# Kernel optimization log

Hardware: AMD Instinct MI355X
Metric: run time of the kernel (lower is better)

Reference implementation:

```python
import jax, jax.numpy as jnp
import numpy as np

B, N, D, H, DD = 4, 256, 768, 12, 64
HD = D // H  # head_dim = 64
SCALE = float(np.sqrt(HD))


def _layernorm(x, g, b, eps=1e-5):
    mu = jnp.mean(x, axis=-1, keepdims=True)
    var = jnp.var(x, axis=-1, keepdims=True)
    return (x - mu) / jnp.sqrt(var + eps) * g + b


def setup_inputs() -> dict:
    key = jax.random.key(0)
    ks = jax.random.split(key, 20)
    def w(k, shape, fan_in):
        return (jax.random.normal(k, shape, jnp.float32) / np.sqrt(fan_in)).astype(jnp.float32)
    x = jax.random.normal(ks[0], (B, N, D), jnp.float32)
    dist = jax.random.normal(ks[1], (B, N, N, DD), jnp.float32)
    mask = jax.random.randint(ks[2], (B, N, N), 0, 2) > 0
    eye = jnp.eye(N, dtype=bool)[None]
    edge_mask = jnp.logical_or(mask, eye)  # guarantee no fully-masked row
    return {
        'x': x, 'distance_features': dist, 'edge_mask': edge_mask,
        'qkv_w': w(ks[3], (D, 3 * D), D), 'qkv_b': jnp.zeros((3 * D,), jnp.float32),
        'out_w': w(ks[4], (D, D), D), 'out_b': jnp.zeros((D,), jnp.float32),
        'rb_w1': w(ks[5], (DD, D), DD), 'rb_b1': jnp.zeros((D,), jnp.float32),
        'rb_w2': w(ks[6], (D, H), D), 'rb_b2': jnp.zeros((H,), jnp.float32),
        'gate_w1': w(ks[7], (D, D), D), 'gate_b1': jnp.zeros((D,), jnp.float32),
        'gate_w2': w(ks[8], (D, D), D), 'gate_b2': jnp.zeros((D,), jnp.float32),
        'ff_w1': w(ks[9], (D, 2 * D), D), 'ff_b1': jnp.zeros((2 * D,), jnp.float32),
        'ff_w2': w(ks[10], (2 * D, D), 2 * D), 'ff_b2': jnp.zeros((D,), jnp.float32),
        'ln1_g': jnp.ones((D,), jnp.float32), 'ln1_b': jnp.zeros((D,), jnp.float32),
        'ln2_g': jnp.ones((D,), jnp.float32), 'ln2_b': jnp.zeros((D,), jnp.float32),
    }


def reference(x, distance_features, edge_mask, qkv_w, qkv_b, out_w, out_b,
              rb_w1, rb_b1, rb_w2, rb_b2, gate_w1, gate_b1, gate_w2, gate_b2,
              ff_w1, ff_b1, ff_w2, ff_b2, ln1_g, ln1_b, ln2_g, ln2_b):
    residual = x
    xn = _layernorm(x, ln1_g, ln1_b)
    qkv = xn @ qkv_w + qkv_b
    q, k, v = jnp.split(qkv, 3, axis=-1)
    q = q.reshape(B, N, H, HD)
    k = k.reshape(B, N, H, HD)
    v = v.reshape(B, N, H, HD)
    logits = jnp.einsum('bihd,bjhd->bhij', q, k) / SCALE
    bias = jax.nn.silu(distance_features @ rb_w1 + rb_b1) @ rb_w2 + rb_b2  # [B,N,N,H]
    logits = logits + jnp.transpose(bias, (0, 3, 1, 2))
    neg = jnp.finfo(logits.dtype).min
    logits = jnp.where(edge_mask[:, None, :, :], logits, neg)
    attn = jax.nn.softmax(logits, axis=-1)
    context = jnp.einsum('bhij,bjhd->bihd', attn, v).reshape(B, N, D)
    gated = jax.nn.silu(xn @ gate_w1 + gate_b1) @ gate_w2 + gate_b2
    x2 = residual + (context * jax.nn.sigmoid(gated)) @ out_w + out_b
    y = _layernorm(x2, ln2_g, ln2_b)
    ff = jax.nn.gelu(y @ ff_w1 + ff_b1, approximate=False) @ ff_w2 + ff_b2
    return x2 + ff
```

## Files before the change

### kernel.cpp

```cpp
#include <hip/hip_runtime.h>
#include <hip/hip_bf16.h>
#include <cmath>

#define U16 unsigned short

typedef __bf16 bf16x8_t __attribute__((ext_vector_type(8)));
typedef float f32x4_t __attribute__((ext_vector_type(4)));

union Frag { uint4 u4; unsigned u[4]; bf16x8_t b8; U16 s[8]; };

__device__ __forceinline__ float b2f(U16 u) {
  union { unsigned int i; float f; } x; x.i = ((unsigned int)u) << 16; return x.f;
}
__device__ __forceinline__ U16 f2b(float f) {
  union { float f; unsigned int i; } x; x.f = f;
  unsigned int r = x.i + 0x7FFFu + ((x.i >> 16) & 1u);
  return (U16)(r >> 16);
}
__device__ __forceinline__ unsigned cvt_pk_bf16(float a, float b) {
  union { __hip_bfloat162 h2; unsigned u; } x;
  x.h2 = __float22bfloat162_rn(make_float2(a, b));
  return x.u;
}
__device__ __forceinline__ float fast_silu(float z) {
  return z * __builtin_amdgcn_rcpf(1.f + __expf(-z));
}
__device__ __forceinline__ void load_lds16(const U16* g, U16* l) {
  __builtin_amdgcn_global_load_lds((const __attribute__((address_space(1))) void*)g,
                                   (__attribute__((address_space(3))) void*)l, 16, 0, 0);
}

__device__ __forceinline__ void ln_row(int row, const float* __restrict__ X,
                                       const float* __restrict__ gam,
                                       const float* __restrict__ bet,
                                       U16* __restrict__ Y) {
  int tid = threadIdx.x, lane = tid & 63, wave = tid >> 6;
  __shared__ float p1[4], p2[4];
  float v[3];
#pragma unroll
  for (int j = 0; j < 3; ++j) v[j] = X[(size_t)row * 768 + tid + j * 256];
  float s1 = v[0] + v[1] + v[2];
  float s2 = v[0] * v[0] + v[1] * v[1] + v[2] * v[2];
#pragma unroll
  for (int m = 32; m > 0; m >>= 1) {
    s1 += __shfl_xor(s1, m);
    s2 += __shfl_xor(s2, m);
  }
  if (lane == 0) { p1[wave] = s1; p2[wave] = s2; }
  __syncthreads();
  float t1 = p1[0] + p1[1] + p1[2] + p1[3];
  float t2 = p2[0] + p2[1] + p2[2] + p2[3];
  float mean = t1 * (1.f / 768.f);
  float var = t2 * (1.f / 768.f) - mean * mean;
  float rstd = rsqrtf(var + 1e-5f);
#pragma unroll
  for (int j = 0; j < 3; ++j) {
    int c = tid + j * 256;
    Y[(size_t)row * 768 + c] = f2b((v[j] - mean) * rstd * gam[c] + bet[c]);
  }
}

__global__ __launch_bounds__(256) void prep_kernel(
    const float* __restrict__ qkv_w, const float* __restrict__ out_w,
    const float* __restrict__ g1w, const float* __restrict__ g2w,
    const float* __restrict__ ff1w, const float* __restrict__ ff2w,
    const float* __restrict__ rb1w, const float* __restrict__ rb2w,
    const float* __restrict__ qkv_b, const float* __restrict__ gate_b1,
    U16* __restrict__ qkv_wT, U16* __restrict__ out_wT, U16* __restrict__ g1wT,
    U16* __restrict__ g2wT, U16* __restrict__ ff1wT, U16* __restrict__ ff2wT,
    U16* __restrict__ rb1wT, U16* __restrict__ rb2wL, float* __restrict__ qg_bias,
    const float* __restrict__ x, const float* __restrict__ ln1_g,
    const float* __restrict__ ln1_b, U16* __restrict__ xn) {
  int bid = blockIdx.x;
  if (bid >= 5868) {
    ln_row(bid - 5868, x, ln1_g, ln1_b, xn);
    return;
  }
  if (bid >= 5856) {
    int idx = (bid - 5856) * 256 + threadIdx.x;
    qg_bias[idx] = (idx < 2304) ? qkv_b[idx] : gate_b1[idx - 2304];
    return;
  }
  if (bid >= 5808) {
    int idx = (bid - 5808) * 256 + threadIdx.x;
    int j = idx & 7, lane = (idx >> 3) & 63, pp = idx >> 9;
    int row = lane & 15, col = pp * 32 + ((lane >> 4) << 3) + j;
    rb2wL[idx] = (row < 12) ? f2b(rb2w[col * 12 + row]) : (U16)0;
    return;
  }
  const float* in; U16* out; int R, C, base;
  if (bid < 1728)      { in = qkv_w; out = qkv_wT; R = 768;  C = 2304; base = 0; }
  else if (bid < 2304) { in = out_w; out = out_wT; R = 768;  C = 768;  base = 1728; }
  else if (bid < 2880) { in = g1w;   out = g1wT;   R = 768;  C = 768;  base = 2304; }
  else if (bid < 3456) { in = g2w;   out = g2wT;   R = 768;  C = 768;  base = 2880; }
  else if (bid < 4608) { in = ff1w;  out = ff1wT;  R = 768;  C = 1536; base = 3456; }
  else if (bid < 5760) { in = ff2w;  out = ff2wT;  R = 1536; C = 768;  base = 4608; }
  else                 { in = rb1w;  out = rb1wT;  R = 64;   C = 768;  base = 5760; }
  int bx = bid - base, tilesx = C / 32;
  int c0 = (bx % tilesx) * 32, r0 = (bx / tilesx) * 32;
  __shared__ float tile[32][33];
  int tx = threadIdx.x & 31, ty = threadIdx.x >> 5;
#pragma unroll
  for (int yy = 0; yy < 4; ++yy)
    tile[ty + yy * 8][tx] = in[(size_t)(r0 + ty + yy * 8) * C + c0 + tx];
  __syncthreads();
#pragma unroll
  for (int yy = 0; yy < 4; ++yy)
    out[(size_t)(c0 + ty + yy * 8) * R + r0 + tx] = f2b(tile[tx][ty + yy * 8]);
}

template <int EPI, bool OUTF32>
__device__ __forceinline__ void gemm_core(U16* sA, U16* sB,
                                          const U16* __restrict__ A,
                                          const U16* __restrict__ BT,
                                          const float* __restrict__ bias,
                                          const float* __restrict__ other,
                                          void* __restrict__ Cout,
                                          float* __restrict__ Cout2,
                                          int N, int K, int bx, int by) {
  int tid = threadIdx.x;
  int lane = tid & 63, wave = tid >> 6;
  int m0 = by * 64, n0 = bx * 64;
  int wm = (wave >> 1) * 32, wn = (wave & 1) * 32;
  int lm = lane & 15, lq = lane >> 4;
  int srow = tid >> 2, scol = (tid & 3) * 8;
  const U16* ag = A + (size_t)(m0 + srow) * K + scol;
  const U16* bg = BT + (size_t)(n0 + srow) * K + scol;
  int nit = K >> 5;
  load_lds16(ag, sA + tid * 8);
  load_lds16(bg, sB + tid * 8);
  f32x4_t acc[2][2] = {};
  for (int i = 0; i < nit; ++i) {
    __syncthreads();
    int cb = (i & 1) * 2048, nb = ((i + 1) & 1) * 2048;
    if (i + 1 < nit) {
      load_lds16(ag + (i + 1) * 32, sA + nb + tid * 8);
      load_lds16(bg + (i + 1) * 32, sB + nb + tid * 8);
    }
    Frag af[2], bf[2];
#pragma unroll
    for (int mt = 0; mt < 2; ++mt)
      af[mt].u4 = *(const uint4*)&sA[cb + (wm + mt * 16 + lm) * 32 + lq * 8];
#pragma unroll
    for (int nt = 0; nt < 2; ++nt)
      bf[nt].u4 = *(const uint4*)&sB[cb + (wn + nt * 16 + lm) * 32 + lq * 8];
#pragma unroll
    for (int mt = 0; mt < 2; ++mt)
#pragma unroll
      for (int nt = 0; nt < 2; ++nt)
        acc[mt][nt] = __builtin_amdgcn_mfma_f32_16x16x32_bf16(af[mt].b8, bf[nt].b8,
                                                              acc[mt][nt], 0, 0, 0);
  }
#pragma unroll
  for (int nt = 0; nt < 2; ++nt) {
    int gc = n0 + wn + nt * 16 + lm;
    float bz = bias[gc];
#pragma unroll
    for (int mt = 0; mt < 2; ++mt) {
#pragma unroll
      for (int r = 0; r < 4; ++r) {
        int gr = m0 + wm + mt * 16 + lq * 4 + r;
        float z = acc[mt][nt][r] + bz;
        if (EPI == 5) {
          if (gc < 2304) Cout2[(size_t)gr * 2304 + gc] = z;
          else ((U16*)Cout)[(size_t)gr * 768 + gc - 2304] = f2b(fast_silu(z));
          continue;
        }
        size_t idx = (size_t)gr * N + gc;
        float o;
        if (EPI == 0) o = z;
        else if (EPI == 2) o = 0.5f * z * (1.f + erff(z * 0.70710678118f));
        else if (EPI == 6) o = __builtin_amdgcn_rcpf(1.f + __expf(-z));
        else o = z + other[idx];
        if (OUTF32) ((float*)Cout)[idx] = o;
        else ((U16*)Cout)[idx] = f2b(o);
      }
    }
  }
}

template <int EPI, bool OUTF32>
__global__ __launch_bounds__(256) void gemm_bt(const U16* __restrict__ A,
                                               const U16* __restrict__ BT,
                                               const float* __restrict__ bias,
                                               const float* __restrict__ other,
                                               void* __restrict__ Cout,
                                               int N, int K) {
  __shared__ __align__(16) U16 sA[2 * 2048];
  __shared__ __align__(16) U16 sB[2 * 2048];
  gemm_core<EPI, OUTF32>(sA, sB, A, BT, bias, other, Cout, nullptr, N, K,
                         blockIdx.x, blockIdx.y);
}

__device__ void rb_body(int bid, const float* __restrict__ dist,
                        const U16* __restrict__ w1T, const float* __restrict__ b1,
                        const U16* __restrict__ w2L, const float* __restrict__ b2,
                        float* __restrict__ biasOut) {
  int tid = threadIdx.x;
  int lane = tid & 63, wave = tid >> 6;
  int lm = lane & 15, lq = lane >> 4;
  int r0 = bid * 512;
  float hb = (lm < 12) ? b2[lm] : 0.f;
  Frag bd[8][2];
#pragma unroll
  for (int g = 0; g < 8; ++g) {
    const float* ap = dist + (size_t)(r0 + (wave * 8 + g) * 16 + lm) * 64 + lq * 8;
    float4 v0 = ((const float4*)ap)[0];
    float4 v1 = ((const float4*)ap)[1];
    float4 v2 = ((const float4*)(ap + 32))[0];
    float4 v3 = ((const float4*)(ap + 32))[1];
    bd[g][0].u[0] = cvt_pk_bf16(v0.x, v0.y); bd[g][0].u[1] = cvt_pk_bf16(v0.z, v0.w);
    bd[g][0].u[2] = cvt_pk_bf16(v1.x, v1.y); bd[g][0].u[3] = cvt_pk_bf16(v1.z, v1.w);
    bd[g][1].u[0] = cvt_pk_bf16(v2.x, v2.y); bd[g][1].u[1] = cvt_pk_bf16(v2.z, v2.w);
    bd[g][1].u[2] = cvt_pk_bf16(v3.x, v3.y); bd[g][1].u[3] = cvt_pk_bf16(v3.z, v3.w);
  }
  const U16* w1p0 = w1T + (size_t)(((lm >> 2) << 3) + (lm & 3)) * 64 + lq * 8;
  const U16* w1p1 = w1p0 + 256;
  const U16* w2p = w2L + lane * 8;
  const float* b1p = b1 + lq * 8;
  f32x4_t bacc[8];
#pragma unroll
  for (int g = 0; g < 8; ++g) bacc[g] = {hb, hb, hb, hb};

  auto loadw = [&](int j, Frag& f00, Frag& f01, Frag& f10, Frag& f11, Frag& fwb,
                   float4& fb0, float4& fb1) {
    const U16* p0 = w1p0 + (size_t)j * 2048;
    const U16* p1 = w1p1 + (size_t)j * 2048;
    f00.u4 = *(const uint4*)p0;
    f01.u4 = *(const uint4*)(p0 + 32);
    f10.u4 = *(const uint4*)p1;
    f11.u4 = *(const uint4*)(p1 + 32);
    fwb.u4 = *(const uint4*)(w2p + (size_t)j * 512);
    fb0 = *(const float4*)(b1p + j * 32);
    fb1 = *(const float4*)(b1p + j * 32 + 4);
  };
  auto comp = [&](Frag& f00, Frag& f01, Frag& f10, Frag& f11, Frag& fwb,
                  float4 fb0, float4 fb1) {
    f32x4_t cz0 = {fb0.x, fb0.y, fb0.z, fb0.w};
    f32x4_t cz1 = {fb1.x, fb1.y, fb1.z, fb1.w};
#pragma unroll
    for (int g = 0; g < 8; ++g) {
      f32x4_t z0 = cz0, z1 = cz1;
      z0 = __builtin_amdgcn_mfma_f32_16x16x32_bf16(f00.b8, bd[g][0].b8, z0, 0, 0, 0);
      z0 = __builtin_amdgcn_mfma_f32_16x16x32_bf16(f01.b8, bd[g][1].b8, z0, 0, 0, 0);
      z1 = __builtin_amdgcn_mfma_f32_16x16x32_bf16(f10.b8, bd[g][0].b8, z1, 0, 0, 0);
      z1 = __builtin_amdgcn_mfma_f32_16x16x32_bf16(f11.b8, bd[g][1].b8, z1, 0, 0, 0);
      float s0 = fast_silu(z0[0]), s1 = fast_silu(z0[1]);
      float s2 = fast_silu(z0[2]), s3 = fast_silu(z0[3]);
      float t0 = fast_silu(z1[0]), t1 = fast_silu(z1[1]);
      float t2 = fast_silu(z1[2]), t3 = fast_silu(z1[3]);
      Frag af2;
      af2.u[0] = cvt_pk_bf16(s0, s1); af2.u[1] = cvt_pk_bf16(s2, s3);
      af2.u[2] = cvt_pk_bf16(t0, t1); af2.u[3] = cvt_pk_bf16(t2, t3);
      bacc[g] = __builtin_amdgcn_mfma_f32_16x16x32_bf16(af2.b8, fwb.b8, bacc[g], 0, 0, 0);
    }
  };

  Frag e00, e01, e10, e11, ewb, o00, o01, o10, o11, owb;
  float4 eb0, eb1, ob0, ob1;
  loadw(0, e00, e01, e10, e11, ewb, eb0, eb1);
  for (int pp = 0; pp < 24; pp += 2) {
    loadw(pp + 1, o00, o01, o10, o11, owb, ob0, ob1);
    comp(e00, e01, e10, e11, ewb, eb0, eb1);
    if (pp + 2 < 24) loadw(pp + 2, e00, e01, e10, e11, ewb, eb0, eb1);
    comp(o00, o01, o10, o11, owb, ob0, ob1);
  }
  if (lm < 12) {
#pragma unroll
    for (int g = 0; g < 8; ++g) {
#pragma unroll
      for (int r = 0; r < 4; ++r) {
        int gr = r0 + (wave * 8 + g) * 16 + lq * 4 + r;
        int b = gr >> 16, rem = gr & 65535, i = rem >> 8, j = rem & 255;
        biasOut[(((size_t)b * 12 + lm) * 256 + i) * 256 + j] = bacc[g][r];
      }
    }
  }
}

__global__ __launch_bounds__(256) void qkvrb_kernel(
    const U16* __restrict__ xn, const U16* __restrict__ qg_wT,
    const float* __restrict__ qg_b, float* __restrict__ qkvb, U16* __restrict__ g1,
    const float* __restrict__ dist, const U16* __restrict__ rb1wT,
    const float* __restrict__ rb_b1, const U16* __restrict__ rb2wL,
    const float* __restrict__ rb_b2, float* __restrict__ biasB) {
  __shared__ __align__(16) U16 sA[2 * 2048];
  __shared__ __align__(16) U16 sB[2 * 2048];
  int bid = blockIdx.x;
  if (bid < 512) {
    rb_body(bid, dist, rb1wT, rb_b1, rb2wL, rb_b2, biasB);
  } else {
    int g = bid - 512;
    gemm_core<5, false>(sA, sB, xn, qg_wT, qg_b, nullptr, g1, qkvb, 3072, 768,
                        g % 48, g / 48);
  }
}

__device__ void attn_body(unsigned char* smem, int bid,
                          const float* __restrict__ qkv,
                          const float* __restrict__ biasB,
                          const int* __restrict__ mask,
                          float* __restrict__ ctx) {
  U16* sK = (U16*)smem;
  float(*sQ)[66] = (float(*)[66])(smem + 33024);
  float* sP = (float*)(smem + 33024 + 4224);
  int tid = threadIdx.x, lane = tid & 63, w = tid >> 6;
  int bh = bid >> 4, b = bh / 12, h = bh % 12;
  int i0 = (bid & 15) * 16;
  {
    int r = tid >> 4, c = (tid & 15) * 4;
    *(float4*)&sQ[r][c] =
        *(const float4*)&qkv[((size_t)(b * 256 + i0 + r)) * 2304 + h * 64 + c];
  }
  {
    const float* kr = qkv + ((size_t)(b * 256 + w * 64)) * 2304 + 768 + h * 64 + lane;
#pragma unroll 8
    for (int rr = 0; rr < 64; ++rr) {
      float kv = kr[(size_t)rr * 2304];
      sK[lane * 258 + w * 64 + rr] = (U16)cvt_pk_bf16(kv, kv);
    }
  }
  __syncthreads();
  int iw = i0 + w * 4;
  float lacc[4][4] = {};
#pragma unroll 4
  for (int d = 0; d < 64; ++d) {
    float k0 = b2f(sK[d * 258 + lane]);
    float k1 = b2f(sK[d * 258 + 64 + lane]);
    float k2 = b2f(sK[d * 258 + 128 + lane]);
    float k3 = b2f(sK[d * 258 + 192 + lane]);
#pragma unroll
    for (int qi = 0; qi < 4; ++qi) {
      float qv = sQ[w * 4 + qi][d];
      lacc[qi][0] += qv * k0;
      lacc[qi][1] += qv * k1;
      lacc[qi][2] += qv * k2;
      lacc[qi][3] += qv * k3;
    }
  }
#pragma unroll
  for (int qi = 0; qi < 4; ++qi) {
    int gi = iw + qi;
    const float* brow = biasB + (((size_t)b * 12 + h) * 256 + gi) * 256;
    const int* mrow = mask + ((size_t)b * 256 + gi) * 256;
    float lg[4];
#pragma unroll
    for (int jc = 0; jc < 4; ++jc) {
      float lv = lacc[qi][jc] * 0.125f + brow[jc * 64 + lane];
      lg[jc] = mrow[jc * 64 + lane] ? lv : -1e30f;
    }
    float mx = fmaxf(fmaxf(lg[0], lg[1]), fmaxf(lg[2], lg[3]));
#pragma unroll
    for (int m = 32; m > 0; m >>= 1) mx = fmaxf(mx, __shfl_xor(mx, m));
    float e[4], sum = 0.f;
#pragma unroll
    for (int jc = 0; jc < 4; ++jc) { e[jc] = __expf(lg[jc] - mx); sum += e[jc]; }
#pragma unroll
    for (int m = 32; m > 0; m >>= 1) sum += __shfl_xor(sum, m);
    float inv = __builtin_amdgcn_rcpf(sum);
#pragma unroll
    for (int jc = 0; jc < 4; ++jc) sP[(w * 4 + qi) * 256 + jc * 64 + lane] = e[jc] * inv;
  }
  float ca[4] = {0.f, 0.f, 0.f, 0.f};
  const float* vcol = qkv + (size_t)b * 256 * 2304 + 1536 + h * 64 + lane;
#pragma unroll 2
  for (int j4 = 0; j4 < 256; j4 += 4) {
    float4 p0 = *(const float4*)&sP[(w * 4 + 0) * 256 + j4];
    float4 p1 = *(const float4*)&sP[(w * 4 + 1) * 256 + j4];
    float4 p2 = *(const float4*)&sP[(w * 4 + 2) * 256 + j4];
    float4 p3 = *(const float4*)&sP[(w * 4 + 3) * 256 + j4];
    const float* pp0 = (const float*)&p0;
    const float* pp1 = (const float*)&p1;
    const float* pp2 = (const float*)&p2;
    const float* pp3 = (const float*)&p3;
#pragma unroll
    for (int jj = 0; jj < 4; ++jj) {
      float v = vcol[(size_t)(j4 + jj) * 2304];
      ca[0] += pp0[jj] * v;
      ca[1] += pp1[jj] * v;
      ca[2] += pp2[jj] * v;
      ca[3] += pp3[jj] * v;
    }
  }
#pragma unroll
  for (int qi = 0; qi < 4; ++qi)
    ctx[((size_t)(b * 256 + iw + qi)) * 768 + h * 64 + lane] = ca[qi];
}

__global__ __launch_bounds__(256) void attn_gate_kernel(
    const float* __restrict__ qkv, const float* __restrict__ biasB,
    const int* __restrict__ mask, float* __restrict__ ctx,
    const U16* __restrict__ g1, const U16* __restrict__ g2wT,
    const float* __restrict__ gate_b2, U16* __restrict__ sg) {
  __shared__ __align__(16) unsigned char smem[53632];
  int bid = blockIdx.x;
  if (bid < 768) {
    attn_body(smem, bid, qkv, biasB, mask, ctx);
  } else {
    int g = bid - 768;
    gemm_core<6, false>((U16*)smem, (U16*)(smem + 8192), g1, g2wT, gate_b2, nullptr,
                        sg, nullptr, 768, 768, g % 12, g / 12);
  }
}

__global__ __launch_bounds__(256) void outp_kernel(const float* __restrict__ ctx,
                                                   const U16* __restrict__ sg,
                                                   const U16* __restrict__ out_wT,
                                                   const float* __restrict__ out_b,
                                                   const float* __restrict__ x,
                                                   float* __restrict__ x2) {
  __shared__ __align__(16) U16 sA[64 * 32];
  __shared__ __align__(16) U16 sB[2 * 2048];
  int tid = threadIdx.x;
  int lane = tid & 63, wave = tid >> 6;
  int m0 = blockIdx.y * 64, n0 = blockIdx.x * 64;
  int wm = (wave >> 1) * 32, wn = (wave & 1) * 32;
  int lm = lane & 15, lq = lane >> 4;
  int srow = tid >> 2, scol = (tid & 3) * 8;
  const float* cg0 = ctx + (size_t)(m0 + srow) * 768 + scol;
  const U16* sg0 = sg + (size_t)(m0 + srow) * 768 + scol;
  const U16* bg = out_wT + (size_t)(n0 + srow) * 768 + scol;
  load_lds16(bg, sB + tid * 8);
  float4 ca0 = *(const float4*)cg0;
  float4 ca1 = *(const float4*)(cg0 + 4);
  Frag sa; sa.u4 = *(const uint4*)sg0;
  f32x4_t acc[2][2] = {};
  for (int i = 0; i < 24; ++i) {
    __syncthreads();
    int cb = (i & 1) * 2048, nb = ((i + 1) & 1) * 2048;
    if (i + 1 < 24) load_lds16(bg + (i + 1) * 32, sB + nb + tid * 8);
    Frag av;
    av.u[0] = cvt_pk_bf16(ca0.x * b2f(sa.s[0]), ca0.y * b2f(sa.s[1]));
    av.u[1] = cvt_pk_bf16(ca0.z * b2f(sa.s[2]), ca0.w * b2f(sa.s[3]));
    av.u[2] = cvt_pk_bf16(ca1.x * b2f(sa.s[4]), ca1.y * b2f(sa.s[5]));
    av.u[3] = cvt_pk_bf16(ca1.z * b2f(sa.s[6]), ca1.w * b2f(sa.s[7]));
    *(uint4*)&sA[tid * 8] = av.u4;
    if (i + 1 < 24) {
      ca0 = *(const float4*)(cg0 + (i + 1) * 32);
      ca1 = *(const float4*)(cg0 + (i + 1) * 32 + 4);
      sa.u4 = *(const uint4*)(sg0 + (i + 1) * 32);
    }
    __syncthreads();
    Frag af[2], bf[2];
#pragma unroll
    for (int mt = 0; mt < 2; ++mt)
      af[mt].u4 = *(const uint4*)&sA[(wm + mt * 16 + lm) * 32 + lq * 8];
#pragma unroll
    for (int nt = 0; nt < 2; ++nt)
      bf[nt].u4 = *(const uint4*)&sB[cb + (wn + nt * 16 + lm) * 32 + lq * 8];
#pragma unroll
    for (int mt = 0; mt < 2; ++mt)
#pragma unroll
      for (int nt = 0; nt < 2; ++nt)
        acc[mt][nt] = __builtin_amdgcn_mfma_f32_16x16x32_bf16(af[mt].b8, bf[nt].b8,
                                                              acc[mt][nt], 0, 0, 0);
  }
#pragma unroll
  for (int nt = 0; nt < 2; ++nt) {
    int gc = n0 + wn + nt * 16 + lm;
    float bz = out_b[gc];
#pragma unroll
    for (int mt = 0; mt < 2; ++mt) {
#pragma unroll
      for (int r = 0; r < 4; ++r) {
        int gr = m0 + wm + mt * 16 + lq * 4 + r;
        size_t idx = (size_t)gr * 768 + gc;
        x2[idx] = acc[mt][nt][r] + bz + x[idx];
      }
    }
  }
}

__global__ __launch_bounds__(256) void ln_kernel(const float* __restrict__ X,
                                                 const float* __restrict__ gam,
                                                 const float* __restrict__ bet,
                                                 U16* __restrict__ Y) {
  ln_row(blockIdx.x, X, gam, bet, Y);
}

extern "C" void kernel_launch(void* const* d_in, const int* in_sizes, int n_in,
                              void* d_out, int out_size, void* d_ws, size_t ws_size,
                              hipStream_t stream) {
  const float* x       = (const float*)d_in[0];
  const float* dist    = (const float*)d_in[1];
  const int* mask      = (const int*)d_in[2];
  const float* qkv_w   = (const float*)d_in[3];
  const float* qkv_b   = (const float*)d_in[4];
  const float* out_w   = (const float*)d_in[5];
  const float* out_b   = (const float*)d_in[6];
  const float* rb_w1   = (const float*)d_in[7];
  const float* rb_b1   = (const float*)d_in[8];
  const float* rb_w2   = (const float*)d_in[9];
  const float* rb_b2   = (const float*)d_in[10];
  const float* gate_w1 = (const float*)d_in[11];
  const float* gate_b1 = (const float*)d_in[12];
  const float* gate_w2 = (const float*)d_in[13];
  const float* gate_b2 = (const float*)d_in[14];
  const float* ff_w1   = (const float*)d_in[15];
  const float* ff_b1   = (const float*)d_in[16];
  const float* ff_w2   = (const float*)d_in[17];
  const float* ff_b2   = (const float*)d_in[18];
  const float* ln1_g   = (const float*)d_in[19];
  const float* ln1_b   = (const float*)d_in[20];
  const float* ln2_g   = (const float*)d_in[21];
  const float* ln2_b   = (const float*)d_in[22];

  char* w = (char*)d_ws;
  auto alloc = [&](size_t bytes) {
    char* p = w;
    w += (bytes + 255) & ~(size_t)255;
    return p;
  };
  U16* xn      = (U16*)alloc(1024 * 768 * 2);
  float* qkvb  = (float*)alloc((size_t)1024 * 2304 * 4);
  U16* qg_wT   = (U16*)alloc((size_t)3072 * 768 * 2);
  U16* qkv_wT  = qg_wT;
  U16* g1wT    = qg_wT + (size_t)2304 * 768;
  float* qg_b  = (float*)alloc(3072 * 4);
  U16* out_wT  = (U16*)alloc(768 * 768 * 2);
  U16* g2wT    = (U16*)alloc(768 * 768 * 2);
  U16* ff1wT   = (U16*)alloc(1536 * 768 * 2);
  U16* ff2wT   = (U16*)alloc(768 * 1536 * 2);
  U16* rb1wT   = (U16*)alloc(768 * 64 * 2);
  U16* rb2wL   = (U16*)alloc(24 * 64 * 8 * 2);
  float* biasB = (float*)alloc((size_t)4 * 12 * 256 * 256 * 4);
  float* ctx   = (float*)alloc(1024 * 768 * 4);
  U16* g1      = (U16*)alloc(1024 * 768 * 2);
  U16* sg      = (U16*)alloc(1024 * 768 * 2);
  float* x2    = (float*)alloc(1024 * 768 * 4);
  U16* y       = (U16*)alloc(1024 * 768 * 2);
  U16* f1      = (U16*)alloc(1024 * 1536 * 2);
  (void)ws_size; (void)in_sizes; (void)n_in; (void)out_size;

  prep_kernel<<<6892, 256, 0, stream>>>(qkv_w, out_w, gate_w1, gate_w2, ff_w1, ff_w2,
                                        rb_w1, rb_w2, qkv_b, gate_b1,
                                        qkv_wT, out_wT, g1wT, g2wT, ff1wT, ff2wT,
                                        rb1wT, rb2wL, qg_b, x, ln1_g, ln1_b, xn);
  qkvrb_kernel<<<1280, 256, 0, stream>>>(xn, qg_wT, qg_b, qkvb, g1,
                                         dist, rb1wT, rb_b1, rb2wL, rb_b2, biasB);
  attn_gate_kernel<<<960, 256, 0, stream>>>(qkvb, biasB, mask, ctx,
                                            g1, g2wT, gate_b2, sg);
  outp_kernel<<<dim3(12, 16), 256, 0, stream>>>(ctx, sg, out_wT, out_b, x, x2);
  ln_kernel<<<1024, 256, 0, stream>>>(x2, ln2_g, ln2_b, y);
  gemm_bt<2, false><<<dim3(24, 16), 256, 0, stream>>>(y, ff1wT, ff_b1, nullptr, f1,
                                                      1536, 768);
  gemm_bt<4, true><<<dim3(12, 16), 256, 0, stream>>>(f1, ff2wT, ff_b2, x2, (float*)d_out,
                                                     768, 1536);
}
```

Measured before the change: 318.2 us.

## Fuse all stages into a persistent megakernel with global atomic barriers

Replaces the seven separate kernel launches with one persistent kernel of 512 blocks. The blocks loop over each stage's work items and meet at software grid barriers built from atomic counters that are zeroed by a memset before the launch. This removes per-launch overhead and the idle gaps between kernels. In exchange it adds spin-wait barriers, and it depends on all 512 blocks being resident at once (two blocks per CU at 53 KB of LDS), otherwise it deadlocks. Later stages with few work items leave many blocks idle, and the restrict qualifiers are dropped.

```diff
diff --git a/kernel.cpp b/kernel.cpp
--- a/kernel.cpp
+++ b/kernel.cpp
@@ -30,12 +30,24 @@
                                    (__attribute__((address_space(3))) void*)l, 16, 0, 0);
 }
 
-__device__ __forceinline__ void ln_row(int row, const float* __restrict__ X,
-                                       const float* __restrict__ gam,
-                                       const float* __restrict__ bet,
-                                       U16* __restrict__ Y) {
+__device__ __forceinline__ void gbar(unsigned* cnt, int idx, unsigned nb) {
+  __syncthreads();
+  if (threadIdx.x == 0) {
+    __threadfence();
+    atomicAdd(&cnt[idx * 16], 1u);
+    while (__hip_atomic_load(&cnt[idx * 16], __ATOMIC_RELAXED,
+                             __HIP_MEMORY_SCOPE_AGENT) < nb)
+      __builtin_amdgcn_s_sleep(2);
+    __threadfence();
+  }
+  __syncthreads();
+}
+
+__device__ __forceinline__ void ln_row(int row, const float* X, const float* gam,
+                                       const float* bet, U16* Y) {
   int tid = threadIdx.x, lane = tid & 63, wave = tid >> 6;
   __shared__ float p1[4], p2[4];
+  __syncthreads();
   float v[3];
 #pragma unroll
   for (int j = 0; j < 3; ++j) v[j] = X[(size_t)row * 768 + tid + j * 256];
@@ -60,22 +72,15 @@
   }
 }
 
-__global__ __launch_bounds__(256) void prep_kernel(
-    const float* __restrict__ qkv_w, const float* __restrict__ out_w,
-    const float* __restrict__ g1w, const float* __restrict__ g2w,
-    const float* __restrict__ ff1w, const float* __restrict__ ff2w,
-    const float* __restrict__ rb1w, const float* __restrict__ rb2w,
-    const float* __restrict__ qkv_b, const float* __restrict__ gate_b1,
-    U16* __restrict__ qkv_wT, U16* __restrict__ out_wT, U16* __restrict__ g1wT,
-    U16* __restrict__ g2wT, U16* __restrict__ ff1wT, U16* __restrict__ ff2wT,
-    U16* __restrict__ rb1wT, U16* __restrict__ rb2wL, float* __restrict__ qg_bias,
-    const float* __restrict__ x, const float* __restrict__ ln1_g,
-    const float* __restrict__ ln1_b, U16* __restrict__ xn) {
-  int bid = blockIdx.x;
-  if (bid >= 5868) {
-    ln_row(bid - 5868, x, ln1_g, ln1_b, xn);
-    return;
-  }
+__device__ void prep_item(int bid, float* tile,
+                          const float* qkv_w, const float* out_w, const float* g1w,
+                          const float* g2w, const float* ff1w, const float* ff2w,
+                          const float* rb1w, const float* rb2w, const float* qkv_b,
+                          const float* gate_b1, U16* qkv_wT, U16* out_wT, U16* g1wT,
+                          U16* g2wT, U16* ff1wT, U16* ff2wT, U16* rb1wT, U16* rb2wL,
+                          float* qg_bias, const float* x, const float* ln1_g,
+                          const float* ln1_b, U16* xn) {
+  if (bid >= 5868) { ln_row(bid - 5868, x, ln1_g, ln1_b, xn); return; }
   if (bid >= 5856) {
     int idx = (bid - 5856) * 256 + threadIdx.x;
     qg_bias[idx] = (idx < 2304) ? qkv_b[idx] : gate_b1[idx - 2304];
@@ -98,26 +103,22 @@
   else                 { in = rb1w;  out = rb1wT;  R = 64;   C = 768;  base = 5760; }
   int bx = bid - base, tilesx = C / 32;
   int c0 = (bx % tilesx) * 32, r0 = (bx / tilesx) * 32;
-  __shared__ float tile[32][33];
   int tx = threadIdx.x & 31, ty = threadIdx.x >> 5;
+  __syncthreads();
 #pragma unroll
   for (int yy = 0; yy < 4; ++yy)
-    tile[ty + yy * 8][tx] = in[(size_t)(r0 + ty + yy * 8) * C + c0 + tx];
+    tile[(ty + yy * 8) * 33 + tx] = in[(size_t)(r0 + ty + yy * 8) * C + c0 + tx];
   __syncthreads();
 #pragma unroll
   for (int yy = 0; yy < 4; ++yy)
-    out[(size_t)(c0 + ty + yy * 8) * R + r0 + tx] = f2b(tile[tx][ty + yy * 8]);
+    out[(size_t)(c0 + ty + yy * 8) * R + r0 + tx] = f2b(tile[tx * 33 + ty + yy * 8]);
 }
 
 template <int EPI, bool OUTF32>
-__device__ __forceinline__ void gemm_core(U16* sA, U16* sB,
-                                          const U16* __restrict__ A,
-                                          const U16* __restrict__ BT,
-                                          const float* __restrict__ bias,
-                                          const float* __restrict__ other,
-                                          void* __restrict__ Cout,
-                                          float* __restrict__ Cout2,
-                                          int N, int K, int bx, int by) {
+__device__ void gemm_core(U16* sA, U16* sB,
+                          const U16* A, const U16* BT, const float* bias,
+                          const float* other, void* Cout, float* Cout2,
+                          int N, int K, int bx, int by) {
   int tid = threadIdx.x;
   int lane = tid & 63, wave = tid >> 6;
   int m0 = by * 64, n0 = bx * 64;
@@ -127,6 +128,7 @@
   const U16* ag = A + (size_t)(m0 + srow) * K + scol;
   const U16* bg = BT + (size_t)(n0 + srow) * K + scol;
   int nit = K >> 5;
+  __syncthreads();
   load_lds16(ag, sA + tid * 8);
   load_lds16(bg, sB + tid * 8);
   f32x4_t acc[2][2] = {};
@@ -179,23 +181,8 @@
   }
 }
 
-template <int EPI, bool OUTF32>
-__global__ __launch_bounds__(256) void gemm_bt(const U16* __restrict__ A,
-                                               const U16* __restrict__ BT,
-                                               const float* __restrict__ bias,
-                                               const float* __restrict__ other,
-                                               void* __restrict__ Cout,
-                                               int N, int K) {
-  __shared__ __align__(16) U16 sA[2 * 2048];
-  __shared__ __align__(16) U16 sB[2 * 2048];
-  gemm_core<EPI, OUTF32>(sA, sB, A, BT, bias, other, Cout, nullptr, N, K,
-                         blockIdx.x, blockIdx.y);
-}
-
-__device__ void rb_body(int bid, const float* __restrict__ dist,
-                        const U16* __restrict__ w1T, const float* __restrict__ b1,
-                        const U16* __restrict__ w2L, const float* __restrict__ b2,
-                        float* __restrict__ biasOut) {
+__device__ void rb_body(int bid, const float* dist, const U16* w1T, const float* b1,
+                        const U16* w2L, const float* b2, float* biasOut) {
   int tid = threadIdx.x;
   int lane = tid & 63, wave = tid >> 6;
   int lm = lane & 15, lq = lane >> 4;
@@ -278,35 +265,15 @@
   }
 }
 
-__global__ __launch_bounds__(256) void qkvrb_kernel(
-    const U16* __restrict__ xn, const U16* __restrict__ qg_wT,
-    const float* __restrict__ qg_b, float* __restrict__ qkvb, U16* __restrict__ g1,
-    const float* __restrict__ dist, const U16* __restrict__ rb1wT,
-    const float* __restrict__ rb_b1, const U16* __restrict__ rb2wL,
-    const float* __restrict__ rb_b2, float* __restrict__ biasB) {
-  __shared__ __align__(16) U16 sA[2 * 2048];
-  __shared__ __align__(16) U16 sB[2 * 2048];
-  int bid = blockIdx.x;
-  if (bid < 512) {
-    rb_body(bid, dist, rb1wT, rb_b1, rb2wL, rb_b2, biasB);
-  } else {
-    int g = bid - 512;
-    gemm_core<5, false>(sA, sB, xn, qg_wT, qg_b, nullptr, g1, qkvb, 3072, 768,
-                        g % 48, g / 48);
-  }
-}
-
-__device__ void attn_body(unsigned char* smem, int bid,
-                          const float* __restrict__ qkv,
-                          const float* __restrict__ biasB,
-                          const int* __restrict__ mask,
-                          float* __restrict__ ctx) {
+__device__ void attn_body(unsigned char* smem, int bid, const float* qkv,
+                          const float* biasB, const int* mask, float* ctx) {
   U16* sK = (U16*)smem;
   float(*sQ)[66] = (float(*)[66])(smem + 33024);
   float* sP = (float*)(smem + 33024 + 4224);
   int tid = threadIdx.x, lane = tid & 63, w = tid >> 6;
   int bh = bid >> 4, b = bh / 12, h = bh % 12;
   int i0 = (bid & 15) * 16;
+  __syncthreads();
   {
     int r = tid >> 4, c = (tid & 15) * 4;
     *(float4*)&sQ[r][c] =
@@ -387,39 +354,21 @@
     ctx[((size_t)(b * 256 + iw + qi)) * 768 + h * 64 + lane] = ca[qi];
 }
 
-__global__ __launch_bounds__(256) void attn_gate_kernel(
-    const float* __restrict__ qkv, const float* __restrict__ biasB,
-    const int* __restrict__ mask, float* __restrict__ ctx,
-    const U16* __restrict__ g1, const U16* __restrict__ g2wT,
-    const float* __restrict__ gate_b2, U16* __restrict__ sg) {
-  __shared__ __align__(16) unsigned char smem[53632];
-  int bid = blockIdx.x;
-  if (bid < 768) {
-    attn_body(smem, bid, qkv, biasB, mask, ctx);
-  } else {
-    int g = bid - 768;
-    gemm_core<6, false>((U16*)smem, (U16*)(smem + 8192), g1, g2wT, gate_b2, nullptr,
-                        sg, nullptr, 768, 768, g % 12, g / 12);
-  }
-}
-
-__global__ __launch_bounds__(256) void outp_kernel(const float* __restrict__ ctx,
-                                                   const U16* __restrict__ sg,
-                                                   const U16* __restrict__ out_wT,
-                                                   const float* __restrict__ out_b,
-                                                   const float* __restrict__ x,
-                                                   float* __restrict__ x2) {
-  __shared__ __align__(16) U16 sA[64 * 32];
-  __shared__ __align__(16) U16 sB[2 * 2048];
+__device__ void outp_body(unsigned char* smem, int bx, int by, const float* ctx,
+                          const U16* sg, const U16* out_wT, const float* out_b,
+                          const float* x, float* x2) {
+  U16* sA = (U16*)smem;
+  U16* sB = (U16*)(smem + 4096);
   int tid = threadIdx.x;
   int lane = tid & 63, wave = tid >> 6;
-  int m0 = blockIdx.y * 64, n0 = blockIdx.x * 64;
+  int m0 = by * 64, n0 = bx * 64;
   int wm = (wave >> 1) * 32, wn = (wave & 1) * 32;
   int lm = lane & 15, lq = lane >> 4;
   int srow = tid >> 2, scol = (tid & 3) * 8;
   const float* cg0 = ctx + (size_t)(m0 + srow) * 768 + scol;
   const U16* sg0 = sg + (size_t)(m0 + srow) * 768 + scol;
   const U16* bg = out_wT + (size_t)(n0 + srow) * 768 + scol;
+  __syncthreads();
   load_lds16(bg, sB + tid * 8);
   float4 ca0 = *(const float4*)cg0;
   float4 ca1 = *(const float4*)(cg0 + 4);
@@ -471,11 +420,59 @@
   }
 }
 
-__global__ __launch_bounds__(256) void ln_kernel(const float* __restrict__ X,
-                                                 const float* __restrict__ gam,
-                                                 const float* __restrict__ bet,
-                                                 U16* __restrict__ Y) {
-  ln_row(blockIdx.x, X, gam, bet, Y);
+__global__ __launch_bounds__(256, 2) void mega_kernel(
+    const float* x, const float* dist, const int* mask,
+    const float* qkv_w, const float* qkv_b, const float* out_w, const float* out_b,
+    const float* rb_w1, const float* rb_b1, const float* rb_w2, const float* rb_b2,
+    const float* gate_w1, const float* gate_b1, const float* gate_w2,
+    const float* gate_b2, const float* ff_w1, const float* ff_b1, const float* ff_w2,
+    const float* ff_b2, const float* ln1_g, const float* ln1_b, const float* ln2_g,
+    const float* ln2_b,
+    U16* xn, float* qkvb, U16* qg_wT, float* qg_b, U16* out_wT, U16* g2wT,
+    U16* ff1wT, U16* ff2wT, U16* rb1wT, U16* rb2wL, float* biasB, float* ctx,
+    U16* g1, U16* sg, float* x2, U16* y, U16* f1, unsigned* counters, float* dout) {
+  __shared__ __align__(16) unsigned char smem[53632];
+  const unsigned NB = 512;
+  U16* g1wT = qg_wT + (size_t)2304 * 768;
+
+  for (int it = blockIdx.x; it < 6892; it += NB)
+    prep_item(it, (float*)smem, qkv_w, out_w, gate_w1, gate_w2, ff_w1, ff_w2, rb_w1,
+              rb_w2, qkv_b, gate_b1, qg_wT, out_wT, g1wT, g2wT, ff1wT, ff2wT, rb1wT,
+              rb2wL, qg_b, x, ln1_g, ln1_b, xn);
+  gbar(counters, 0, NB);
+  for (int it = blockIdx.x; it < 1280; it += NB) {
+    if (it < 512) {
+      rb_body(it, dist, rb1wT, rb_b1, rb2wL, rb_b2, biasB);
+    } else {
+      int g = it - 512;
+      gemm_core<5, false>((U16*)smem, (U16*)(smem + 8192), xn, qg_wT, qg_b, nullptr,
+                          g1, qkvb, 3072, 768, g % 48, g / 48);
+    }
+  }
+  gbar(counters, 1, NB);
+  for (int it = blockIdx.x; it < 960; it += NB) {
+    if (it < 768) {
+      attn_body(smem, it, qkvb, biasB, mask, ctx);
+    } else {
+      int g = it - 768;
+      gemm_core<6, false>((U16*)smem, (U16*)(smem + 8192), g1, g2wT, gate_b2, nullptr,
+                          sg, nullptr, 768, 768, g % 12, g / 12);
+    }
+  }
+  gbar(counters, 2, NB);
+  for (int it = blockIdx.x; it < 192; it += NB)
+    outp_body(smem, it % 12, it / 12, ctx, sg, out_wT, out_b, x, x2);
+  gbar(counters, 3, NB);
+  for (int it = blockIdx.x; it < 1024; it += NB)
+    ln_row(it, x2, ln2_g, ln2_b, y);
+  gbar(counters, 4, NB);
+  for (int it = blockIdx.x; it < 384; it += NB)
+    gemm_core<2, false>((U16*)smem, (U16*)(smem + 8192), y, ff1wT, ff_b1, nullptr,
+                        f1, nullptr, 1536, 768, it % 24, it / 24);
+  gbar(counters, 5, NB);
+  for (int it = blockIdx.x; it < 192; it += NB)
+    gemm_core<4, true>((U16*)smem, (U16*)(smem + 8192), f1, ff2wT, ff_b2, x2, dout,
+                       nullptr, 768, 1536, it % 12, it / 12);
 }
 
 extern "C" void kernel_launch(void* const* d_in, const int* in_sizes, int n_in,
@@ -511,11 +508,10 @@
     w += (bytes + 255) & ~(size_t)255;
     return p;
   };
+  unsigned* counters = (unsigned*)alloc(512);
   U16* xn      = (U16*)alloc(1024 * 768 * 2);
   float* qkvb  = (float*)alloc((size_t)1024 * 2304 * 4);
   U16* qg_wT   = (U16*)alloc((size_t)3072 * 768 * 2);
-  U16* qkv_wT  = qg_wT;
-  U16* g1wT    = qg_wT + (size_t)2304 * 768;
   float* qg_b  = (float*)alloc(3072 * 4);
   U16* out_wT  = (U16*)alloc(768 * 768 * 2);
   U16* g2wT    = (U16*)alloc(768 * 768 * 2);
@@ -532,18 +528,11 @@
   U16* f1      = (U16*)alloc(1024 * 1536 * 2);
   (void)ws_size; (void)in_sizes; (void)n_in; (void)out_size;
 
-  prep_kernel<<<6892, 256, 0, stream>>>(qkv_w, out_w, gate_w1, gate_w2, ff_w1, ff_w2,
-                                        rb_w1, rb_w2, qkv_b, gate_b1,
-                                        qkv_wT, out_wT, g1wT, g2wT, ff1wT, ff2wT,
-                                        rb1wT, rb2wL, qg_b, x, ln1_g, ln1_b, xn);
-  qkvrb_kernel<<<1280, 256, 0, stream>>>(xn, qg_wT, qg_b, qkvb, g1,
-                                         dist, rb1wT, rb_b1, rb2wL, rb_b2, biasB);
-  attn_gate_kernel<<<960, 256, 0, stream>>>(qkvb, biasB, mask, ctx,
-                                            g1, g2wT, gate_b2, sg);
-  outp_kernel<<<dim3(12, 16), 256, 0, stream>>>(ctx, sg, out_wT, out_b, x, x2);
-  ln_kernel<<<1024, 256, 0, stream>>>(x2, ln2_g, ln2_b, y);
-  gemm_bt<2, false><<<dim3(24, 16), 256, 0, stream>>>(y, ff1wT, ff_b1, nullptr, f1,
-                                                      1536, 768);
-  gemm_bt<4, true><<<dim3(12, 16), 256, 0, stream>>>(f1, ff2wT, ff_b2, x2, (float*)d_out,
-                                                     768, 1536);
-}
+  hipMemsetAsync(counters, 0, 512, stream);
+  mega_kernel<<<512, 256, 0, stream>>>(
+      x, dist, mask, qkv_w, qkv_b, out_w, out_b, rb_w1, rb_b1, rb_w2, rb_b2,
+      gate_w1, gate_b1, gate_w2, gate_b2, ff_w1, ff_b1, ff_w2, ff_b2,
+      ln1_g, ln1_b, ln2_g, ln2_b,
+      xn, qkvb, qg_wT, qg_b, out_wT, g2wT, ff1wT, ff2wT, rb1wT, rb2wL,
+      biasB, ctx, g1, sg, x2, y, f1, counters, (float*)d_out);
+}
```

Measured after the change: 613.1 us. +92.7%, slower.

## Fuse tail stages into one persistent kernel with global atomic barriers

Applied to the files above, without the earlier changes.

Merges the output projection, second layernorm, and both feed-forward GEMMs into a single persistent kernel of 384 blocks. The stages are separated by software grid barriers built from atomic counters, which are zeroed by a memset before each run. The goal is to remove three kernel launch gaps and their ramp-up and drain. The cost is that the barriers spin on atomics, and the kernel can deadlock if all 384 blocks are not resident at once. Some stages also use fewer than 384 blocks, so the remaining blocks sit idle at the barrier.

```diff
diff --git a/kernel.cpp b/kernel.cpp
--- a/kernel.cpp
+++ b/kernel.cpp
@@ -28,6 +28,19 @@
 __device__ __forceinline__ void load_lds16(const U16* g, U16* l) {
   __builtin_amdgcn_global_load_lds((const __attribute__((address_space(1))) void*)g,
                                    (__attribute__((address_space(3))) void*)l, 16, 0, 0);
+}
+
+__device__ __forceinline__ void gbar(unsigned* cnt, int idx, unsigned nb) {
+  __syncthreads();
+  if (threadIdx.x == 0) {
+    __threadfence();
+    atomicAdd(&cnt[idx * 16], 1u);
+    while (__hip_atomic_load(&cnt[idx * 16], __ATOMIC_RELAXED,
+                             __HIP_MEMORY_SCOPE_AGENT) < nb)
+      __builtin_amdgcn_s_sleep(32);
+    __threadfence();
+  }
+  __syncthreads();
 }
 
 __device__ __forceinline__ void ln_row(int row, const float* __restrict__ X,
@@ -36,6 +49,7 @@
                                        U16* __restrict__ Y) {
   int tid = threadIdx.x, lane = tid & 63, wave = tid >> 6;
   __shared__ float p1[4], p2[4];
+  __syncthreads();
   float v[3];
 #pragma unroll
   for (int j = 0; j < 3; ++j) v[j] = X[(size_t)row * 768 + tid + j * 256];
@@ -110,14 +124,10 @@
 }
 
 template <int EPI, bool OUTF32>
-__device__ __forceinline__ void gemm_core(U16* sA, U16* sB,
-                                          const U16* __restrict__ A,
-                                          const U16* __restrict__ BT,
-                                          const float* __restrict__ bias,
-                                          const float* __restrict__ other,
-                                          void* __restrict__ Cout,
-                                          float* __restrict__ Cout2,
-                                          int N, int K, int bx, int by) {
+__device__ void gemm_core(U16* sA, U16* sB,
+                          const U16* A, const U16* BT, const float* bias,
+                          const float* other, void* Cout, float* Cout2,
+                          int N, int K, int bx, int by) {
   int tid = threadIdx.x;
   int lane = tid & 63, wave = tid >> 6;
   int m0 = by * 64, n0 = bx * 64;
@@ -179,23 +189,8 @@
   }
 }
 
-template <int EPI, bool OUTF32>
-__global__ __launch_bounds__(256) void gemm_bt(const U16* __restrict__ A,
-                                               const U16* __restrict__ BT,
-                                               const float* __restrict__ bias,
-                                               const float* __restrict__ other,
-                                               void* __restrict__ Cout,
-                                               int N, int K) {
-  __shared__ __align__(16) U16 sA[2 * 2048];
-  __shared__ __align__(16) U16 sB[2 * 2048];
-  gemm_core<EPI, OUTF32>(sA, sB, A, BT, bias, other, Cout, nullptr, N, K,
-                         blockIdx.x, blockIdx.y);
-}
-
-__device__ void rb_body(int bid, const float* __restrict__ dist,
-                        const U16* __restrict__ w1T, const float* __restrict__ b1,
-                        const U16* __restrict__ w2L, const float* __restrict__ b2,
-                        float* __restrict__ biasOut) {
+__device__ void rb_body(int bid, const float* dist, const U16* w1T, const float* b1,
+                        const U16* w2L, const float* b2, float* biasOut) {
   int tid = threadIdx.x;
   int lane = tid & 63, wave = tid >> 6;
   int lm = lane & 15, lq = lane >> 4;
@@ -296,11 +291,8 @@
   }
 }
 
-__device__ void attn_body(unsigned char* smem, int bid,
-                          const float* __restrict__ qkv,
-                          const float* __restrict__ biasB,
-                          const int* __restrict__ mask,
-                          float* __restrict__ ctx) {
+__device__ void attn_body(unsigned char* smem, int bid, const float* qkv,
+                          const float* biasB, const int* mask, float* ctx) {
   U16* sK = (U16*)smem;
   float(*sQ)[66] = (float(*)[66])(smem + 33024);
   float* sP = (float*)(smem + 33024 + 4224);
@@ -403,17 +395,12 @@
   }
 }
 
-__global__ __launch_bounds__(256) void outp_kernel(const float* __restrict__ ctx,
-                                                   const U16* __restrict__ sg,
-                                                   const U16* __restrict__ out_wT,
-                                                   const float* __restrict__ out_b,
-                                                   const float* __restrict__ x,
-                                                   float* __restrict__ x2) {
-  __shared__ __align__(16) U16 sA[64 * 32];
-  __shared__ __align__(16) U16 sB[2 * 2048];
+__device__ void outp_body(U16* sA, U16* sB, int bx, int by, const float* ctx,
+                          const U16* sg, const U16* out_wT, const float* out_b,
+                          const float* x, float* x2) {
   int tid = threadIdx.x;
   int lane = tid & 63, wave = tid >> 6;
-  int m0 = blockIdx.y * 64, n0 = blockIdx.x * 64;
+  int m0 = by * 64, n0 = bx * 64;
   int wm = (wave >> 1) * 32, wn = (wave & 1) * 32;
   int lm = lane & 15, lq = lane >> 4;
   int srow = tid >> 2, scol = (tid & 3) * 8;
@@ -471,11 +458,27 @@
   }
 }
 
-__global__ __launch_bounds__(256) void ln_kernel(const float* __restrict__ X,
-                                                 const float* __restrict__ gam,
-                                                 const float* __restrict__ bet,
-                                                 U16* __restrict__ Y) {
-  ln_row(blockIdx.x, X, gam, bet, Y);
+__global__ __launch_bounds__(256, 2) void tail_kernel(
+    const float* ctx, const U16* sg, const U16* out_wT, const float* out_b,
+    const float* x, float* x2, const float* ln2_g, const float* ln2_b, U16* y,
+    const U16* ff1wT, const float* ff_b1, U16* f1, const U16* ff2wT,
+    const float* ff_b2, float* dout, unsigned* counters) {
+  __shared__ __align__(16) U16 sA[2 * 2048];
+  __shared__ __align__(16) U16 sB[2 * 2048];
+  const unsigned NB = 384;
+  for (int it = blockIdx.x; it < 192; it += NB)
+    outp_body(sA, sB, it % 12, it / 12, ctx, sg, out_wT, out_b, x, x2);
+  gbar(counters, 0, NB);
+  for (int it = blockIdx.x; it < 1024; it += NB)
+    ln_row(it, x2, ln2_g, ln2_b, y);
+  gbar(counters, 1, NB);
+  for (int it = blockIdx.x; it < 384; it += NB)
+    gemm_core<2, false>(sA, sB, y, ff1wT, ff_b1, nullptr, f1, nullptr,
+                        1536, 768, it % 24, it / 24);
+  gbar(counters, 2, NB);
+  for (int it = blockIdx.x; it < 192; it += NB)
+    gemm_core<4, true>(sA, sB, f1, ff2wT, ff_b2, x2, dout, nullptr,
+                       768, 1536, it % 12, it / 12);
 }
 
 extern "C" void kernel_launch(void* const* d_in, const int* in_sizes, int n_in,
@@ -511,6 +514,7 @@
     w += (bytes + 255) & ~(size_t)255;
     return p;
   };
+  unsigned* counters = (unsigned*)alloc(512);
   U16* xn      = (U16*)alloc(1024 * 768 * 2);
   float* qkvb  = (float*)alloc((size_t)1024 * 2304 * 4);
   U16* qg_wT   = (U16*)alloc((size_t)3072 * 768 * 2);
@@ -532,6 +536,7 @@
   U16* f1      = (U16*)alloc(1024 * 1536 * 2);
   (void)ws_size; (void)in_sizes; (void)n_in; (void)out_size;
 
+  hipMemsetAsync(counters, 0, 512, stream);
   prep_kernel<<<6892, 256, 0, stream>>>(qkv_w, out_w, gate_w1, gate_w2, ff_w1, ff_w2,
                                         rb_w1, rb_w2, qkv_b, gate_b1,
                                         qkv_wT, out_wT, g1wT, g2wT, ff1wT, ff2wT,
@@ -540,10 +545,7 @@
                                          dist, rb1wT, rb_b1, rb2wL, rb_b2, biasB);
   attn_gate_kernel<<<960, 256, 0, stream>>>(qkvb, biasB, mask, ctx,
                                             g1, g2wT, gate_b2, sg);
-  outp_kernel<<<dim3(12, 16), 256, 0, stream>>>(ctx, sg, out_wT, out_b, x, x2);
-  ln_kernel<<<1024, 256, 0, stream>>>(x2, ln2_g, ln2_b, y);
-  gemm_bt<2, false><<<dim3(24, 16), 256, 0, stream>>>(y, ff1wT, ff_b1, nullptr, f1,
-                                                      1536, 768);
-  gemm_bt<4, true><<<dim3(12, 16), 256, 0, stream>>>(f1, ff2wT, ff_b2, x2, (float*)d_out,
-                                                     768, 1536);
-}
+  tail_kernel<<<384, 256, 0, stream>>>(ctx, sg, out_wT, out_b, x, x2, ln2_g, ln2_b,
+                                       y, ff1wT, ff_b1, f1, ff2wT, ff_b2,
+                                       (float*)d_out, counters);
+}
```

Measured after the change: 425.9 us. 33.8% more time.
